# Kernel optimization log

Hardware: AMD Instinct MI355X
Metric: run time of the kernel (lower is better)

The kernel has to match this reference:

```python
import jax, jax.numpy as jnp
import numpy as np


def setup_inputs() -> dict:
    key = jax.random.key(0)
    k1, k2, k3 = jax.random.split(key, 3)
    B, D, C = 16384, 1024, 14
    z_image = jax.random.normal(k1, (B, D), dtype=jnp.float32)
    z_text = jax.random.normal(k2, (B, D), dtype=jnp.float32)
    labels = jax.random.randint(k3, (B, C), 0, 2, dtype=jnp.int32)
    return {"z_image": z_image, "z_text": z_text, "labels": labels}


def _margins(labels):
    # labels: [B, C] binary; imposter index j = (i+1) % B -> roll by -1
    lj = jnp.roll(labels, -1, axis=0)
    equal = jnp.all(labels == lj, axis=1)                     # [B]
    n = jnp.sum(labels | lj, axis=1).astype(jnp.float32)      # union size
    d = jnp.sum(labels ^ lj, axis=1).astype(jnp.float32)      # hamming diff
    m = jnp.where(n > 0, jnp.maximum(0.5, d / jnp.maximum(n, 1.0)), 0.5)
    return jnp.where(equal, 0.0, m)                           # [B]


def reference(z_image, z_text, labels):
    # similarity_function == 'dot' (default path of the torch module)
    margin = _margins(labels)                                  # [B]
    paired = jnp.sum(z_image * z_text, axis=1)                 # dot(img_i, txt_i)
    imp_img = jnp.sum(jnp.roll(z_image, -1, axis=0) * z_text, axis=1)  # dot(img_j, txt_i)
    imp_txt = jnp.sum(jnp.roll(z_text, -1, axis=0) * z_image, axis=1)  # dot(txt_j, img_i)
    loss_img = jnp.mean(jax.nn.relu(imp_img - paired + margin))
    loss_txt = jnp.mean(jax.nn.relu(imp_txt - paired + margin))
    return loss_img + loss_txt
```

## Files before the change

### kernel.cpp

```cpp
#include <hip/hip_runtime.h>


constexpr int D = 1024;
constexpr int C = 14;
constexpr int ROWS_PER_BLOCK = 16;
constexpr int WAVES_PER_BLOCK = 4;
constexpr int ROWS_PER_WAVE = ROWS_PER_BLOCK / WAVES_PER_BLOCK;

__global__ __launch_bounds__(256) void ranking_loss_kernel(
    const float* __restrict__ zi, const float* __restrict__ zt,
    const int* __restrict__ labels, float* __restrict__ out, int B)
{
    const int wave = threadIdx.x >> 6;
    const int lane = threadIdx.x & 63;

    float local = 0.0f;

    const int base_row = blockIdx.x * ROWS_PER_BLOCK + wave * ROWS_PER_WAVE;

    for (int k = 0; k < ROWS_PER_WAVE; ++k) {
        const int row = base_row + k;
        int nrow = row + 1;
        if (nrow == B) nrow = 0;

        const float4* zi_r = (const float4*)(zi + (size_t)row  * D);
        const float4* zt_r = (const float4*)(zt + (size_t)row  * D);
        const float4* zi_n = (const float4*)(zi + (size_t)nrow * D);
        const float4* zt_n = (const float4*)(zt + (size_t)nrow * D);

        float paired = 0.0f, imp_img = 0.0f, imp_txt = 0.0f;
        #pragma unroll
        for (int j = 0; j < 4; ++j) {
            const int idx = lane + 64 * j;
            const float4 a  = zi_r[idx];
            const float4 b  = zt_r[idx];
            const float4 an = zi_n[idx];
            const float4 bn = zt_n[idx];
            paired  += a.x*b.x  + a.y*b.y  + a.z*b.z  + a.w*b.w;
            imp_img += an.x*b.x + an.y*b.y + an.z*b.z + an.w*b.w;
            imp_txt += bn.x*a.x + bn.y*a.y + bn.z*a.z + bn.w*a.w;
        }

        float dv = 0.0f, nv = 0.0f;
        if (lane < C) {
            const int li = labels[(size_t)row  * C + lane];
            const int lj = labels[(size_t)nrow * C + lane];
            dv = (float)(li ^ lj);
            nv = (float)(li | lj);
        }

        #pragma unroll
        for (int off = 32; off > 0; off >>= 1) {
            paired  += __shfl_down(paired,  off, 64);
            imp_img += __shfl_down(imp_img, off, 64);
            imp_txt += __shfl_down(imp_txt, off, 64);
            dv      += __shfl_down(dv,      off, 64);
            nv      += __shfl_down(nv,      off, 64);
        }

        if (lane == 0) {
            const float margin =
                (dv == 0.0f) ? 0.0f : fmaxf(0.5f, dv / fmaxf(nv, 1.0f));
            const float t_img = fmaxf(imp_img - paired + margin, 0.0f);
            const float t_txt = fmaxf(imp_txt - paired + margin, 0.0f);
            local += t_img + t_txt;
        }
    }

    __shared__ float smem[WAVES_PER_BLOCK];
    if (lane == 0) smem[wave] = local;
    __syncthreads();
    if (threadIdx.x == 0) {
        float s = 0.0f;
        #pragma unroll
        for (int w = 0; w < WAVES_PER_BLOCK; ++w) s += smem[w];
        atomicAdd(out, s / (float)B);
    }
}

extern "C" void kernel_launch(void* const* d_in, const int* in_sizes, int n_in,
                              void* d_out, int out_size, void* d_ws, size_t ws_size,
                              hipStream_t stream) {
    const float* zi     = (const float*)d_in[0];
    const float* zt     = (const float*)d_in[1];
    const int*   labels = (const int*)d_in[2];
    float*       out    = (float*)d_out;

    const int B = in_sizes[0] / D;

    hipMemsetAsync(out, 0, (size_t)out_size * sizeof(float), stream);

    const int blocks = B / ROWS_PER_BLOCK;
    ranking_loss_kernel<<<blocks, 256, 0, stream>>>(zi, zt, labels, out, B);
}
```

Baseline: 154.2 us.

## Reuse neighbor rows across a wave's rows and replace atomics with two-phase reduction

Each wave now loads its 4 consecutive rows plus one extra neighbor row once and reuses them for both the paired and imposter dot products. Previously each row and its successor were fetched separately, nearly doubling global reads. Label margins are computed for all rows at once with ballot and popcount instead of per-row shuffles. The memset and per-block atomicAdd are replaced by per-block partial sums plus a second single-block reduction kernel. The trade-offs are more registers, an extra launch, and a wraparound using `& (B-1)` that assumes B is a power of two.

```diff
diff --git a/kernel.cpp b/kernel.cpp
--- a/kernel.cpp
+++ b/kernel.cpp
@@ -1,81 +1,110 @@
 #include <hip/hip_runtime.h>
 
 
-constexpr int D = 1024;
-constexpr int C = 14;
-constexpr int ROWS_PER_BLOCK = 16;
-constexpr int WAVES_PER_BLOCK = 4;
-constexpr int ROWS_PER_WAVE = ROWS_PER_BLOCK / WAVES_PER_BLOCK;
+constexpr int D   = 1024;
+constexpr int C   = 14;
+constexpr int RPW = 4;
+constexpr int WPB = 4;
+constexpr int RPB = RPW * WPB;
 
-__global__ __launch_bounds__(256) void ranking_loss_kernel(
+__device__ __forceinline__ float dot4(const float4 x, const float4 y) {
+    return x.x * y.x + x.y * y.y + x.z * y.z + x.w * y.w;
+}
+
+__global__ __launch_bounds__(256) void rank_phase1(
     const float* __restrict__ zi, const float* __restrict__ zt,
-    const int* __restrict__ labels, float* __restrict__ out, int B)
+    const int* __restrict__ labels, float* __restrict__ partial, int B)
 {
     const int wave = threadIdx.x >> 6;
     const int lane = threadIdx.x & 63;
+    const int r0   = blockIdx.x * RPB + wave * RPW;
+    const int M    = B - 1;
 
-    float local = 0.0f;
+    const float4* zi_r[RPW + 1];
+    const float4* zt_r[RPW + 1];
+    #pragma unroll
+    for (int k = 0; k <= RPW; ++k) {
+        const int r = (r0 + k) & M;
+        zi_r[k] = (const float4*)(zi + (size_t)r * D);
+        zt_r[k] = (const float4*)(zt + (size_t)r * D);
+    }
 
-    const int base_row = blockIdx.x * ROWS_PER_BLOCK + wave * ROWS_PER_WAVE;
+    float p [RPW] = {0.f, 0.f, 0.f, 0.f};
+    float ii[RPW] = {0.f, 0.f, 0.f, 0.f};
+    float it[RPW] = {0.f, 0.f, 0.f, 0.f};
 
-    for (int k = 0; k < ROWS_PER_WAVE; ++k) {
-        const int row = base_row + k;
-        int nrow = row + 1;
-        if (nrow == B) nrow = 0;
-
-        const float4* zi_r = (const float4*)(zi + (size_t)row  * D);
-        const float4* zt_r = (const float4*)(zt + (size_t)row  * D);
-        const float4* zi_n = (const float4*)(zi + (size_t)nrow * D);
-        const float4* zt_n = (const float4*)(zt + (size_t)nrow * D);
-
-        float paired = 0.0f, imp_img = 0.0f, imp_txt = 0.0f;
+    #pragma unroll
+    for (int j = 0; j < 4; ++j) {
+        const int idx = lane + 64 * j;
+        float4 a[RPW + 1], b[RPW + 1];
         #pragma unroll
-        for (int j = 0; j < 4; ++j) {
-            const int idx = lane + 64 * j;
-            const float4 a  = zi_r[idx];
-            const float4 b  = zt_r[idx];
-            const float4 an = zi_n[idx];
-            const float4 bn = zt_n[idx];
-            paired  += a.x*b.x  + a.y*b.y  + a.z*b.z  + a.w*b.w;
-            imp_img += an.x*b.x + an.y*b.y + an.z*b.z + an.w*b.w;
-            imp_txt += bn.x*a.x + bn.y*a.y + bn.z*a.z + bn.w*a.w;
-        }
-
-        float dv = 0.0f, nv = 0.0f;
-        if (lane < C) {
-            const int li = labels[(size_t)row  * C + lane];
-            const int lj = labels[(size_t)nrow * C + lane];
-            dv = (float)(li ^ lj);
-            nv = (float)(li | lj);
-        }
-
+        for (int k = 0; k <= RPW; ++k) a[k] = zi_r[k][idx];
         #pragma unroll
-        for (int off = 32; off > 0; off >>= 1) {
-            paired  += __shfl_down(paired,  off, 64);
-            imp_img += __shfl_down(imp_img, off, 64);
-            imp_txt += __shfl_down(imp_txt, off, 64);
-            dv      += __shfl_down(dv,      off, 64);
-            nv      += __shfl_down(nv,      off, 64);
-        }
-
-        if (lane == 0) {
-            const float margin =
-                (dv == 0.0f) ? 0.0f : fmaxf(0.5f, dv / fmaxf(nv, 1.0f));
-            const float t_img = fmaxf(imp_img - paired + margin, 0.0f);
-            const float t_txt = fmaxf(imp_txt - paired + margin, 0.0f);
-            local += t_img + t_txt;
+        for (int k = 0; k <= RPW; ++k) b[k] = zt_r[k][idx];
+        #pragma unroll
+        for (int k = 0; k < RPW; ++k) {
+            p [k] += dot4(a[k],     b[k]);
+            ii[k] += dot4(a[k + 1], b[k]);
+            it[k] += dot4(b[k + 1], a[k]);
         }
     }
 
-    __shared__ float smem[WAVES_PER_BLOCK];
+    const int kk = lane >> 4;
+    const int c  = lane & 15;
+    int lx = 0, lo = 0;
+    if (c < C) {
+        const int ra = (r0 + kk)     & M;
+        const int rb = (r0 + kk + 1) & M;
+        const int li = labels[(size_t)ra * C + c];
+        const int lj = labels[(size_t)rb * C + c];
+        lx = li ^ lj;
+        lo = li | lj;
+    }
+    const unsigned long long bx = __ballot(lx != 0);
+    const unsigned long long bo = __ballot(lo != 0);
+
+    #pragma unroll
+    for (int off = 32; off > 0; off >>= 1) {
+        #pragma unroll
+        for (int k = 0; k < RPW; ++k) {
+            p [k] += __shfl_down(p [k], off, 64);
+            ii[k] += __shfl_down(ii[k], off, 64);
+            it[k] += __shfl_down(it[k], off, 64);
+        }
+    }
+
+    float local = 0.f;
+    if (lane == 0) {
+        #pragma unroll
+        for (int k = 0; k < RPW; ++k) {
+            const float dv = (float)__popcll((bx >> (16 * k)) & 0x3FFFull);
+            const float nv = (float)__popcll((bo >> (16 * k)) & 0x3FFFull);
+            const float m  = (dv == 0.f) ? 0.f : fmaxf(0.5f, dv / nv);
+            local += fmaxf(ii[k] - p[k] + m, 0.f)
+                   + fmaxf(it[k] - p[k] + m, 0.f);
+        }
+    }
+
+    __shared__ float smem[WPB];
     if (lane == 0) smem[wave] = local;
     __syncthreads();
-    if (threadIdx.x == 0) {
-        float s = 0.0f;
-        #pragma unroll
-        for (int w = 0; w < WAVES_PER_BLOCK; ++w) s += smem[w];
-        atomicAdd(out, s / (float)B);
-    }
+    if (threadIdx.x == 0)
+        partial[blockIdx.x] = smem[0] + smem[1] + smem[2] + smem[3];
+}
+
+__global__ __launch_bounds__(256) void rank_phase2(
+    const float* __restrict__ partial, float* __restrict__ out,
+    int npart, float invB)
+{
+    float s = 0.f;
+    for (int i = threadIdx.x; i < npart; i += 256) s += partial[i];
+    #pragma unroll
+    for (int off = 32; off > 0; off >>= 1) s += __shfl_down(s, off, 64);
+    __shared__ float sm[4];
+    if ((threadIdx.x & 63) == 0) sm[threadIdx.x >> 6] = s;
+    __syncthreads();
+    if (threadIdx.x == 0)
+        out[0] = (sm[0] + sm[1] + sm[2] + sm[3]) * invB;
 }
 
 extern "C" void kernel_launch(void* const* d_in, const int* in_sizes, int n_in,
@@ -85,11 +114,11 @@
     const float* zt     = (const float*)d_in[1];
     const int*   labels = (const int*)d_in[2];
     float*       out    = (float*)d_out;
+    float*       ws     = (float*)d_ws;
 
-    const int B = in_sizes[0] / D;
+    const int B      = in_sizes[0] / D;
+    const int blocks = B / RPB;
 
-    hipMemsetAsync(out, 0, (size_t)out_size * sizeof(float), stream);
-
-    const int blocks = B / ROWS_PER_BLOCK;
-    ranking_loss_kernel<<<blocks, 256, 0, stream>>>(zi, zt, labels, out, B);
+    rank_phase1<<<blocks, 256, 0, stream>>>(zi, zt, labels, ws, B);
+    rank_phase2<<<1, 256, 0, stream>>>(ws, out, blocks, 1.0f / (float)B);
 }
```

Result: faster. 150.0 us (-2.7%).
